# Optimization experiments

Measured on AMD Instinct MI355X. Metric: run time of the kernel, lower is better.

Reference implementation:

```python
import jax, jax.numpy as jnp
import numpy as np

TEMPERATURE = 0.07


def setup_inputs() -> dict:
    key = jax.random.key(0)
    k1, k2 = jax.random.split(key)
    B, V, D = 4096, 5, 512
    img = jax.random.normal(k1, (B, D), dtype=jnp.float32)
    txt = jax.random.normal(k2, (B, V, D), dtype=jnp.float32)
    # module assumes pre-normalized features
    img = img / jnp.linalg.norm(img, axis=-1, keepdims=True)
    txt = txt / jnp.linalg.norm(txt, axis=-1, keepdims=True)
    return {"image_features": img, "text_features_all": txt}


def reference(image_features, text_features_all):
    B, V, D = text_features_all.shape
    text_flat = text_features_all.reshape(B * V, D)          # (BV, D)
    logits = (image_features @ text_flat.T) / TEMPERATURE    # (B, BV)

    # i2t: per image-row, soft targets = 1/V on its V positive texts
    row_lse = jax.nn.logsumexp(logits, axis=1)               # (B,)
    pos_logits = logits.reshape(B, B, V)[jnp.arange(B), jnp.arange(B)]  # (B, V)
    loss_i2t = jnp.mean(row_lse - jnp.mean(pos_logits, axis=1))

    # t2i: per text-column, cross-entropy over B images, target = col // V
    col_lse = jax.nn.logsumexp(logits, axis=0)               # (BV,)
    img_idx = jnp.arange(B * V) // V
    pos_col = logits[img_idx, jnp.arange(B * V)]             # (BV,)
    loss_t2i = jnp.mean(col_lse - pos_col)

    return (loss_i2t + loss_t2i) * 0.5
```

## Files before the change

### kernel.cpp

```cpp
#include <hip/hip_runtime.h>
#include <stdint.h>

#define B_  4096
#define V_  5
#define D_  512
#define NN_ (B_ * V_)
#define NBLK_ 5120

#define C_EXP 20.609929155556620f
#define M_SHIFT (1.0f / 0.07f)
#define SCALE1 0x7f7f7f7f

typedef float floatx4 __attribute__((ext_vector_type(4)));
typedef int   intx4   __attribute__((ext_vector_type(4)));
typedef int   intx8   __attribute__((ext_vector_type(8)));

__device__ __forceinline__ void load_lds16(const void* g, void* l) {
  __builtin_amdgcn_global_load_lds(
      (const __attribute__((address_space(1))) unsigned int*)g,
      (__attribute__((address_space(3))) unsigned int*)l,
      16, 0, 0);
}

__global__ void cvt_kernel(const float* __restrict__ img, const float* __restrict__ txt,
                           uint8_t* __restrict__ out8, float* __restrict__ acc) {
  const int t = blockIdx.x * 256 + threadIdx.x;
  if (t < B_ + NN_) acc[t] = 0.0f;
  const float4* src; int g;
  if (t < (B_ * D_) / 16) { src = (const float4*)img; g = t; }
  else                    { src = (const float4*)txt; g = t - (B_ * D_) / 16; }
  float4 a = src[4 * g + 0], b = src[4 * g + 1];
  float4 c = src[4 * g + 2], d = src[4 * g + 3];
  int w0 = __builtin_amdgcn_cvt_pk_fp8_f32(a.x, a.y, 0, 0);
  w0     = __builtin_amdgcn_cvt_pk_fp8_f32(a.z, a.w, w0, 1);
  int w1 = __builtin_amdgcn_cvt_pk_fp8_f32(b.x, b.y, 0, 0);
  w1     = __builtin_amdgcn_cvt_pk_fp8_f32(b.z, b.w, w1, 1);
  int w2 = __builtin_amdgcn_cvt_pk_fp8_f32(c.x, c.y, 0, 0);
  w2     = __builtin_amdgcn_cvt_pk_fp8_f32(c.z, c.w, w2, 1);
  int w3 = __builtin_amdgcn_cvt_pk_fp8_f32(d.x, d.y, 0, 0);
  w3     = __builtin_amdgcn_cvt_pk_fp8_f32(d.z, d.w, w3, 1);
  ((int4*)out8)[t] = make_int4(w0, w1, w2, w3);
}

__global__ __launch_bounds__(256, 2)
void gemm_kernel(const uint8_t* __restrict__ Ah, const uint8_t* __restrict__ Bh,
                 float* __restrict__ row_sum, float* __restrict__ col_sum,
                 float* __restrict__ posPart) {
  __shared__ __align__(16) uint8_t As[2][2 * 128 * 64];
  __shared__ __align__(16) uint8_t Bs[2][2 * 128 * 64];
  const int tid  = threadIdx.x;
  const int lane = tid & 63;
  const int w    = tid >> 6;
  const int wm   = w >> 1, wn = w & 1;
  const int m0   = blockIdx.x * 128;
  const int n0   = blockIdx.y * 128;

  floatx4 acc[4][4] = {};

  const int sc = ((lane & 3) ^ ((lane >> 3) & 3)) * 16;
  const uint8_t* gA = Ah + (size_t)(m0 + w * 32 + (lane >> 2)) * D_ + sc;
  const uint8_t* gB = Bh + (size_t)(n0 + w * 32 + (lane >> 2)) * D_ + sc;
  const int lofs = (w * 32) * 64;

  const int fr  = lane & 15;
  const int swz = (fr >> 1) & 3;
  const int qb  = (lane >> 5) & 1;
  const int qh  = (lane >> 4) & 1;
  const int c0  = ((qh * 2 + 0) ^ swz) * 16;
  const int c1  = ((qh * 2 + 1) ^ swz) * 16;
  const int bufo = qb * 8192;

  #define STAGE(s, A, B) do {                                      \
    const int kg = (s) * 128;                                      \
    load_lds16(gA + kg,                (A) + lofs);                \
    load_lds16(gA + kg + 16 * D_,      (A) + lofs + 16 * 64);      \
    load_lds16(gB + kg,                (B) + lofs);                \
    load_lds16(gB + kg + 16 * D_,      (B) + lofs + 16 * 64);      \
    load_lds16(gA + kg + 64,           (A) + 8192 + lofs);         \
    load_lds16(gA + kg + 64 + 16 * D_, (A) + 8192 + lofs + 16 * 64); \
    load_lds16(gB + kg + 64,           (B) + 8192 + lofs);         \
    load_lds16(gB + kg + 64 + 16 * D_, (B) + 8192 + lofs + 16 * 64); \
  } while (0)

  STAGE(0, As[0], Bs[0]);

  for (int ss = 0; ss < 4; ++ss) {
    const int p = ss & 1;
    __syncthreads();

    if (ss < 3) STAGE(ss + 1, As[1 - p], Bs[1 - p]);

    intx8 af[4], bf[4];
#pragma unroll
    for (int f = 0; f < 4; ++f) {
      const uint8_t* Ar = As[p] + bufo + (wm * 64 + f * 16 + fr) * 64;
      const uint8_t* Br = Bs[p] + bufo + (wn * 64 + f * 16 + fr) * 64;
      intx4 alo = *(const intx4*)(Ar + c0);
      intx4 ahi = *(const intx4*)(Ar + c1);
      intx4 blo = *(const intx4*)(Br + c0);
      intx4 bhi = *(const intx4*)(Br + c1);
      af[f] = __builtin_shufflevector(alo, ahi, 0, 1, 2, 3, 4, 5, 6, 7);
      bf[f] = __builtin_shufflevector(blo, bhi, 0, 1, 2, 3, 4, 5, 6, 7);
    }

#pragma unroll
    for (int mf = 0; mf < 4; ++mf)
#pragma unroll
      for (int nf = 0; nf < 4; ++nf)
        acc[mf][nf] = __builtin_amdgcn_mfma_scale_f32_16x16x128_f8f6f4(
            af[mf], bf[nf], acc[mf][nf],
            0, 0,
            0, SCALE1,
            0, SCALE1);
  }
  #undef STAGE

  {
    float ps = 0.0f;
    const int iLo = n0 / 5, iHi = (n0 + 127) / 5;
    if (iHi >= m0 && iLo < m0 + 128) {
      const int rbase = m0 + wm * 64 + ((lane >> 4) << 2);
#pragma unroll
      for (int nf = 0; nf < 4; ++nf) {
        const int ci = (n0 + wn * 64 + nf * 16 + (lane & 15)) / 5;
#pragma unroll
        for (int mf = 0; mf < 4; ++mf)
#pragma unroll
          for (int r = 0; r < 4; ++r)
            if (rbase + mf * 16 + r == ci) ps += acc[mf][nf][r];
      }
    }
    for (int o = 32; o; o >>= 1) ps += __shfl_xor(ps, o);
    __shared__ float pls[4];
    if (lane == 0) pls[w] = ps;
    __syncthreads();
    if (tid == 0)
      posPart[blockIdx.y * 32 + blockIdx.x] = pls[0] + pls[1] + pls[2] + pls[3];
  }

#pragma unroll
  for (int mf = 0; mf < 4; ++mf)
#pragma unroll
    for (int nf = 0; nf < 4; ++nf)
#pragma unroll
      for (int r = 0; r < 4; ++r)
        acc[mf][nf][r] = exp2f(acc[mf][nf][r] * C_EXP - C_EXP);

  float cs[4];
#pragma unroll
  for (int nf = 0; nf < 4; ++nf) {
    float s = 0.0f;
#pragma unroll
    for (int mf = 0; mf < 4; ++mf)
      s += acc[mf][nf][0] + acc[mf][nf][1] + acc[mf][nf][2] + acc[mf][nf][3];
    s += __shfl_xor(s, 16);
    s += __shfl_xor(s, 32);
    cs[nf] = s;
  }
  {
    int g = lane >> 4;
    float v = (g == 0) ? cs[0] : (g == 1) ? cs[1] : (g == 2) ? cs[2] : cs[3];
    atomicAdd(&col_sum[n0 + wn * 64 + (g << 4) + (lane & 15)], v);
  }

#pragma unroll
  for (int mf = 0; mf < 4; ++mf) {
    floatx4 t = acc[mf][0] + acc[mf][1] + acc[mf][2] + acc[mf][3];
#pragma unroll
    for (int r = 0; r < 4; ++r) {
      float s = t[r];
      s += __shfl_xor(s, 1); s += __shfl_xor(s, 2);
      s += __shfl_xor(s, 4); s += __shfl_xor(s, 8);
      t[r] = s;
    }
    if ((lane & 15) < 4) {
      int q = lane & 3;
      float v = (q == 0) ? t[0] : (q == 1) ? t[1] : (q == 2) ? t[2] : t[3];
      atomicAdd(&row_sum[m0 + wm * 64 + mf * 16 + ((lane >> 4) << 2) + q], v);
    }
  }
}

__global__ void finish_kernel(const float* __restrict__ acc, const float* __restrict__ posPart,
                              float* __restrict__ out) {
  int tid = threadIdx.x;
  float sA = 0.0f, sB = 0.0f, sP = 0.0f;
  for (int i = tid; i < B_;    i += 1024) sA += logf(acc[i]);
  for (int i = tid; i < NN_;   i += 1024) sB += logf(acc[B_ + i]);
  for (int i = tid; i < NBLK_; i += 1024) sP += posPart[i];
  float s = sA * (1.0f / B_) + sB * (1.0f / NN_)
          - sP * (2.0f * M_SHIFT / (float)NN_);
  for (int o = 32; o; o >>= 1) s += __shfl_xor(s, o);
  __shared__ float ls[16];
  int lane = tid & 63, w = tid >> 6;
  if (lane == 0) ls[w] = s;
  __syncthreads();
  if (tid == 0) {
    float tot = 0.0f;
#pragma unroll
    for (int i = 0; i < 16; ++i) tot += ls[i];
    out[0] = M_SHIFT + 0.5f * tot;
  }
}

extern "C" void kernel_launch(void* const* d_in, const int* in_sizes, int n_in,
                              void* d_out, int out_size, void* d_ws, size_t ws_size,
                              hipStream_t stream) {
  const float* img = (const float*)d_in[0];
  const float* txt = (const float*)d_in[1];

  const size_t fp8Bytes = (size_t)(B_ * D_ + NN_ * D_);
  const size_t needBytes = fp8Bytes + (size_t)(B_ + NN_ + NBLK_) * 4;
  if (ws_size < needBytes) return;

  uint8_t* Ah  = (uint8_t*)d_ws;
  uint8_t* Bh  = Ah + (size_t)B_ * D_;
  float* acc   = (float*)((char*)d_ws + fp8Bytes);
  float* row_s = acc;
  float* col_s = acc + B_;
  float* posP  = acc + B_ + NN_;

  cvt_kernel   <<<3072, 256, 0, stream>>>(img, txt, Ah, acc);
  gemm_kernel  <<<dim3(32, 160), 256, 0, stream>>>(Ah, Bh, row_s, col_s, posP);
  finish_kernel<<<1, 1024, 0, stream>>>(acc, posP, (float*)d_out);
}
```

Baseline: 176.9 us.

## Single-buffer LDS tiles and raise occupancy to four blocks per CU

```diff
diff --git a/kernel.cpp b/kernel.cpp
--- a/kernel.cpp
+++ b/kernel.cpp
@@ -42,12 +42,12 @@
   ((int4*)out8)[t] = make_int4(w0, w1, w2, w3);
 }
 
-__global__ __launch_bounds__(256, 2)
+__global__ __launch_bounds__(256, 4)
 void gemm_kernel(const uint8_t* __restrict__ Ah, const uint8_t* __restrict__ Bh,
                  float* __restrict__ row_sum, float* __restrict__ col_sum,
                  float* __restrict__ posPart) {
-  __shared__ __align__(16) uint8_t As[2][2 * 128 * 64];
-  __shared__ __align__(16) uint8_t Bs[2][2 * 128 * 64];
+  __shared__ __align__(16) uint8_t As[2 * 128 * 64];
+  __shared__ __align__(16) uint8_t Bs[2 * 128 * 64];
   const int tid  = threadIdx.x;
   const int lane = tid & 63;
   const int w    = tid >> 6;
@@ -70,31 +70,29 @@
   const int c1  = ((qh * 2 + 1) ^ swz) * 16;
   const int bufo = qb * 8192;
 
-  #define STAGE(s, A, B) do {                                      \
+  #define STAGE(s) do {                                            \
     const int kg = (s) * 128;                                      \
-    load_lds16(gA + kg,                (A) + lofs);                \
-    load_lds16(gA + kg + 16 * D_,      (A) + lofs + 16 * 64);      \
-    load_lds16(gB + kg,                (B) + lofs);                \
-    load_lds16(gB + kg + 16 * D_,      (B) + lofs + 16 * 64);      \
-    load_lds16(gA + kg + 64,           (A) + 8192 + lofs);         \
-    load_lds16(gA + kg + 64 + 16 * D_, (A) + 8192 + lofs + 16 * 64); \
-    load_lds16(gB + kg + 64,           (B) + 8192 + lofs);         \
-    load_lds16(gB + kg + 64 + 16 * D_, (B) + 8192 + lofs + 16 * 64); \
+    load_lds16(gA + kg,                As + lofs);                 \
+    load_lds16(gA + kg + 16 * D_,      As + lofs + 16 * 64);       \
+    load_lds16(gB + kg,                Bs + lofs);                 \
+    load_lds16(gB + kg + 16 * D_,      Bs + lofs + 16 * 64);       \
+    load_lds16(gA + kg + 64,           As + 8192 + lofs);          \
+    load_lds16(gA + kg + 64 + 16 * D_, As + 8192 + lofs + 16 * 64);\
+    load_lds16(gB + kg + 64,           Bs + 8192 + lofs);          \
+    load_lds16(gB + kg + 64 + 16 * D_, Bs + 8192 + lofs + 16 * 64);\
   } while (0)
 
-  STAGE(0, As[0], Bs[0]);
-
+  STAGE(0);
+
+#pragma unroll
   for (int ss = 0; ss < 4; ++ss) {
-    const int p = ss & 1;
     __syncthreads();
 
-    if (ss < 3) STAGE(ss + 1, As[1 - p], Bs[1 - p]);
-
     intx8 af[4], bf[4];
 #pragma unroll
     for (int f = 0; f < 4; ++f) {
-      const uint8_t* Ar = As[p] + bufo + (wm * 64 + f * 16 + fr) * 64;
-      const uint8_t* Br = Bs[p] + bufo + (wn * 64 + f * 16 + fr) * 64;
+      const uint8_t* Ar = As + bufo + (wm * 64 + f * 16 + fr) * 64;
+      const uint8_t* Br = Bs + bufo + (wn * 64 + f * 16 + fr) * 64;
       intx4 alo = *(const intx4*)(Ar + c0);
       intx4 ahi = *(const intx4*)(Ar + c1);
       intx4 blo = *(const intx4*)(Br + c0);
@@ -102,6 +100,10 @@
       af[f] = __builtin_shufflevector(alo, ahi, 0, 1, 2, 3, 4, 5, 6, 7);
       bf[f] = __builtin_shufflevector(blo, bhi, 0, 1, 2, 3, 4, 5, 6, 7);
     }
+
+    __syncthreads();
+
+    if (ss < 3) STAGE(ss + 1);
 
 #pragma unroll
     for (int mf = 0; mf < 4; ++mf)
```

Result: faster. 157.1 us (-11.2%).
